# Kernel optimization log

Hardware: AMD Instinct MI355X
Metric: run time of the kernel (lower is better)

The kernel has to match this reference:

```python
import jax, jax.numpy as jnp
import numpy as np


def setup_inputs() -> dict:
    key0 = jax.random.key(0)
    kq, kk, kv = jax.random.split(key0, 3)
    B, S, H, KVH, D = 1, 4096, 8, 2, 64
    return {
        "query": jax.random.normal(kq, (B, S, H, D), dtype=jnp.float32),
        "key": jax.random.normal(kk, (B, S, KVH, D), dtype=jnp.float32),
        "value": jax.random.normal(kv, (B, S, KVH, D), dtype=jnp.float32),
    }


def _ring_attn_single(query, key, value):
    # world_size == 1 (dist uninitialized): ring loop is a single local step
    # with query_offset == key_offset == 0.
    B, S, H, D = query.shape
    KVH = key.shape[2]
    scale = D ** -0.5
    # [B, H, S, D]
    q = query.transpose(0, 2, 1, 3)
    k = key.transpose(0, 2, 1, 3)
    v = value.transpose(0, 2, 1, 3)
    if KVH != H:
        rep = H // KVH
        k = jnp.repeat(k, rep, axis=1)  # repeat_interleave on head dim
        v = jnp.repeat(v, rep, axis=1)
    logits = jnp.einsum("bhqd,bhkd->bhqk", q, k) * scale
    pos = jnp.arange(S)
    causal = pos[:, None] < pos[None, :]  # mask future keys
    logits = jnp.where(causal[None, None], -jnp.inf, logits)
    w = jax.nn.softmax(logits, axis=-1)  # [B, H, S, S]
    attn_out = jnp.einsum("bhqk,bhkd->bhqd", w, v)
    cw = jnp.sum(w, axis=-1, keepdims=True)  # chunk softmax mass (== 1)
    out = attn_out * cw / (cw + 1e-8)  # weight-accumulation renorm
    return out.transpose(0, 2, 1, 3)  # [B, S, H, D]


def reference(query, key, value):
    return _ring_attn_single(query, key, value)
```

## Files before the change

### kernel.cpp

```cpp
#include <hip/hip_runtime.h>
#include <hip/hip_bf16.h>


#define S_LEN 4096
#define H_Q   8
#define H_KV  2
#define DH    64
#define BN    64
#define NEG_BIG (-1e30f)
#define CS (0.125f * 1.44269504088896340736f)

#define CHUNK 6
#define NTR   187
#define KB_SH (S_LEN * H_KV * DH)
#define TILE_SH 4096
#define KVH_SH  (S_LEN * DH)
#define OB_SH    ((size_t)NTR * H_Q * 128 * DH)
#define L_FLOATS ((size_t)NTR * H_Q * 128)
#define WS_NEED ((size_t)(2 * KB_SH) * 2 + OB_SH * 2 + L_FLOATS * 4)

typedef __attribute__((ext_vector_type(8))) short bf16x8;
typedef __attribute__((ext_vector_type(4))) short s16x4;
typedef __attribute__((ext_vector_type(4))) float f32x4;
typedef __attribute__((ext_vector_type(4))) unsigned int u32x4;

__device__ __forceinline__ short bf(float x) {
    return __builtin_bit_cast(short, __float2bfloat16(x));
}
__device__ __forceinline__ float fbf(short u) {
    return __builtin_bit_cast(float, ((unsigned int)(unsigned short)u) << 16);
}
__device__ __forceinline__ unsigned int cvtpk(float lo, float hi) {
    unsigned int r;
    asm("v_cvt_pk_bf16_f32 %0, %1, %2" : "=v"(r) : "v"(lo), "v"(hi));
    return r;
}
__device__ __forceinline__ void gload16(const short* gp, short* lp) {
    __builtin_amdgcn_global_load_lds(
        (const __attribute__((address_space(1))) unsigned int*)gp,
        (__attribute__((address_space(3))) unsigned int*)lp, 16, 0, 0);
}

__global__ __launch_bounds__(256)
void ring_attn_prepass(const float* __restrict__ K, const float* __restrict__ V,
                       short* __restrict__ Kb, short* __restrict__ Vt) {
    const int b = blockIdx.x;
    const int t = threadIdx.x;
    if (b < 512) {
        const int i = (b * 256 + t) * 4;
        const int s   = i >> 7;
        const int kvh = (i >> 6) & 1;
        const int d   = i & 63;
        float4 kv = *(const float4*)(K + i);
        const int dst = kvh * KVH_SH + (s >> 6) * TILE_SH + (s & 63) * 64
                      + (((d >> 3) ^ (s & 7)) * 8) + (d & 7);
        *(unsigned int*)(Kb + dst)     = cvtpk(kv.x, kv.y);
        *(unsigned int*)(Kb + dst + 2) = cvtpk(kv.z, kv.w);
    } else {
        __shared__ short T[DH * 72];
        const int bb  = b - 512;
        const int kvh = bb >> 6;
        const int j   = bb & 63;
        const int s0  = j * 64;
        {
            const int r  = t >> 2;
            const int dq = (t & 3) * 16;
            const float* vp = V + ((s0 + r) * H_KV + kvh) * DH + dq;
            float4 a0 = *(const float4*)(vp);
            float4 a1 = *(const float4*)(vp + 4);
            float4 a2 = *(const float4*)(vp + 8);
            float4 a3 = *(const float4*)(vp + 12);
            float e[16] = {a0.x,a0.y,a0.z,a0.w, a1.x,a1.y,a1.z,a1.w,
                           a2.x,a2.y,a2.z,a2.w, a3.x,a3.y,a3.z,a3.w};
#pragma unroll
            for (int i2 = 0; i2 < 16; ++i2)
                T[(dq + i2) * 72 + r] = bf(e[i2]);
        }
        __syncthreads();
        {
            const int d = t >> 2;
            const int q = t & 3;
            s16x4 g0 = *(const s16x4*)(&T[d * 72 + 4 * q]);
            s16x4 g1 = *(const s16x4*)(&T[d * 72 + 16 + 4 * q]);
            s16x4 g2 = *(const s16x4*)(&T[d * 72 + 32 + 4 * q]);
            s16x4 g3 = *(const s16x4*)(&T[d * 72 + 48 + 4 * q]);
            bf16x8 x0 = bf16x8{g0[0],g0[1],g0[2],g0[3], g1[0],g1[1],g1[2],g1[3]};
            bf16x8 x1 = bf16x8{g2[0],g2[1],g2[2],g2[3], g3[0],g3[1],g3[2],g3[3]};
            short* base = Vt + kvh * KVH_SH + j * TILE_SH + d * 64;
            *(bf16x8*)(base + ((2 * q)     ^ (d & 7)) * 8) = x0;
            *(bf16x8*)(base + ((2 * q + 1) ^ (d & 7)) * 8) = x1;
        }
    }
}

template <bool SPLIT>
__global__ __launch_bounds__(256, 4)
void ring_attn_fwd(const float* __restrict__ Q, const short* __restrict__ Kb,
                   const short* __restrict__ Vt, float* __restrict__ O,
                   short* __restrict__ Obuf, float* __restrict__ Lbuf) {
    const int bid = blockIdx.x;
    const int h   = bid & 7;
    int qt, nch, jbeg, jend, tr0;
    if (SPLIT) {
        const int tr = (NTR - 1) - (bid >> 3);
        int g = 0, base = 0;
        for (;;) {
            const int cnt2 = ((g == 10) ? 2 : 3) * (g + 1);
            if (tr < base + cnt2) break;
            base += cnt2; ++g;
        }
        const int u  = tr - base;
        const int qq = u / (g + 1);
        const int ch = u - qq * (g + 1);
        qt   = 3 * g + qq;
        nch  = g + 1;
        tr0  = base + qq * (g + 1);
        jbeg = ch * CHUNK;
        jend = min(2 * qt + 2, jbeg + CHUNK);
    } else {
        qt = 31 - (bid >> 3);
        nch = 1; jbeg = 0; jend = 2 * qt + 2; tr0 = 0;
    }
    const int kvh = h >> 2;

    __shared__ short Ksb[2][4096];
    __shared__ short Vsb[2][4096];

    const int tid  = threadIdx.x;
    const int w    = tid >> 6;
    const int lane = tid & 63;
    const int c    = lane & 15;
    const int q    = lane >> 4;
    const int e    = c & 7;

    bf16x8 qf[2][2];
#pragma unroll
    for (int st = 0; st < 2; ++st) {
        const int qg = qt * 128 + st * 64 + w * 16 + c;
        const float* qp = Q + (qg * H_Q + h) * DH + q * 8;
        float4 a0 = *(const float4*)(qp);
        float4 a1 = *(const float4*)(qp + 4);
        float4 b0 = *(const float4*)(qp + 32);
        float4 b1 = *(const float4*)(qp + 36);
        u32x4 u0 = {cvtpk(a0.x*CS, a0.y*CS), cvtpk(a0.z*CS, a0.w*CS),
                    cvtpk(a1.x*CS, a1.y*CS), cvtpk(a1.z*CS, a1.w*CS)};
        u32x4 u1 = {cvtpk(b0.x*CS, b0.y*CS), cvtpk(b0.z*CS, b0.w*CS),
                    cvtpk(b1.x*CS, b1.y*CS), cvtpk(b1.z*CS, b1.w*CS)};
        qf[st][0] = __builtin_bit_cast(bf16x8, u0);
        qf[st][1] = __builtin_bit_cast(bf16x8, u1);
    }

    f32x4 acc[2][4] = {};
    float l_lane[2] = {0.f, 0.f};

    const short* gkb = Kb + kvh * KVH_SH + w * 1024 + lane * 8;
    const short* gvb = Vt + kvh * KVH_SH + w * 1024 + lane * 8;
#define STAGE(buf, j)                                             \
    do {                                                          \
        const short* gk = gkb + (j) * TILE_SH;                    \
        const short* gv = gvb + (j) * TILE_SH;                    \
        short* lk = &Ksb[buf][w * 1024];                          \
        short* lv = &Vsb[buf][w * 1024];                          \
        gload16(gk, lk);        gload16(gk + 512, lk + 512);      \
        gload16(gv, lv);        gload16(gv + 512, lv + 512);      \
    } while (0)

    STAGE(0, jbeg);

    for (int j = jbeg; j < jend; ++j) {
        const int cur = (j - jbeg) & 1;
        __syncthreads();
        if (j + 1 < jend)
            STAGE(cur ^ 1, j + 1);

        const short* Kc = Ksb[cur];
        const short* Vc = Vsb[cur];

        f32x4 s[2][4] = {};
#pragma unroll
        for (int nt = 0; nt < 4; ++nt) {
            const int rb = (nt * 16 + c) * 64;
            bf16x8 kf0 = *(const bf16x8*)(Kc + rb + (q ^ e) * 8);
            bf16x8 kf1 = *(const bf16x8*)(Kc + rb + ((q + 4) ^ e) * 8);
            s[0][nt] = __builtin_amdgcn_mfma_f32_16x16x32_bf16(kf0, qf[0][0], s[0][nt], 0, 0, 0);
            s[0][nt] = __builtin_amdgcn_mfma_f32_16x16x32_bf16(kf1, qf[0][1], s[0][nt], 0, 0, 0);
            s[1][nt] = __builtin_amdgcn_mfma_f32_16x16x32_bf16(kf0, qf[1][0], s[1][nt], 0, 0, 0);
            s[1][nt] = __builtin_amdgcn_mfma_f32_16x16x32_bf16(kf1, qf[1][1], s[1][nt], 0, 0, 0);
        }

        bf16x8 pf[2][2];
#pragma unroll
        for (int st = 0; st < 2; ++st) {
            if (j >= 2 * qt + st) {
                const int koff = (j - 2 * qt - st) * 64;
                const int qrl  = w * 16 + c;
#pragma unroll
                for (int nt = 0; nt < 4; ++nt) {
                    const int kl = koff + nt * 16 + q * 4;
#pragma unroll
                    for (int r = 0; r < 4; ++r)
                        if (kl + r > qrl) s[st][nt][r] = NEG_BIG;
                }
            }
#pragma unroll
            for (int nt = 0; nt < 4; ++nt)
#pragma unroll
                for (int r = 0; r < 4; ++r) {
                    const float p = __builtin_amdgcn_exp2f(s[st][nt][r]);
                    s[st][nt][r] = p;
                    l_lane[st] += p;
                }
            u32x4 w0 = {cvtpk(s[st][0][0], s[st][0][1]), cvtpk(s[st][0][2], s[st][0][3]),
                        cvtpk(s[st][1][0], s[st][1][1]), cvtpk(s[st][1][2], s[st][1][3])};
            u32x4 w1 = {cvtpk(s[st][2][0], s[st][2][1]), cvtpk(s[st][2][2], s[st][2][3]),
                        cvtpk(s[st][3][0], s[st][3][1]), cvtpk(s[st][3][2], s[st][3][3])};
            pf[st][0] = __builtin_bit_cast(bf16x8, w0);
            pf[st][1] = __builtin_bit_cast(bf16x8, w1);
        }

#pragma unroll
        for (int dt = 0; dt < 4; ++dt) {
            const int nb = (dt * 16 + c) * 64;
            bf16x8 vf0 = *(const bf16x8*)(Vc + nb + ((2 * q)     ^ e) * 8);
            bf16x8 vf1 = *(const bf16x8*)(Vc + nb + ((2 * q + 1) ^ e) * 8);
            acc[0][dt] = __builtin_amdgcn_mfma_f32_16x16x32_bf16(pf[0][0], vf0, acc[0][dt], 0, 0, 0);
            acc[0][dt] = __builtin_amdgcn_mfma_f32_16x16x32_bf16(pf[0][1], vf1, acc[0][dt], 0, 0, 0);
            acc[1][dt] = __builtin_amdgcn_mfma_f32_16x16x32_bf16(pf[1][0], vf0, acc[1][dt], 0, 0, 0);
            acc[1][dt] = __builtin_amdgcn_mfma_f32_16x16x32_bf16(pf[1][1], vf1, acc[1][dt], 0, 0, 0);
        }
    }

    float lr[2][4];
#pragma unroll
    for (int st = 0; st < 2; ++st) {
        float t2 = l_lane[st];
        t2 += __shfl_xor(t2, 16);
        t2 += __shfl_xor(t2, 32);
        l_lane[st] = t2;
#pragma unroll
        for (int r = 0; r < 4; ++r)
            lr[st][r] = __shfl(t2, q * 4 + r);
    }

    if (!SPLIT || nch == 1) {
#pragma unroll
        for (int st = 0; st < 2; ++st)
#pragma unroll
            for (int r = 0; r < 4; ++r) {
                const float inv = 1.0f / lr[st][r];
                const int row = qt * 128 + st * 64 + w * 16 + q * 4 + r;
                float* op = O + (row * H_Q + h) * DH + c;
#pragma unroll
                for (int dt = 0; dt < 4; ++dt)
                    op[dt * 16] = acc[st][dt][r] * inv;
            }
    } else {
        const int slot = (tr0 + jbeg / CHUNK) * 8 + h;
        short* ob = Obuf + (size_t)slot * (128 * DH);
#pragma unroll
        for (int st = 0; st < 2; ++st) {
#pragma unroll
            for (int r = 0; r < 4; ++r) {
                const int rin = st * 64 + w * 16 + q * 4 + r;
#pragma unroll
                for (int dt = 0; dt < 4; ++dt)
                    ob[rin * DH + dt * 16 + c] = bf(acc[st][dt][r]);
            }
            if (lane < 16)
                Lbuf[slot * 128 + st * 64 + w * 16 + lane] = l_lane[st];
        }
    }
}

__global__ __launch_bounds__(256)
void ring_attn_combine(const short* __restrict__ Obuf, const float* __restrict__ Lbuf,
                       float* __restrict__ O) {
    const int gid  = blockIdx.x * 256 + threadIdx.x;
    const int d    = gid & 63;
    const int h    = (gid >> 6) & 7;
    const int srow = 384 + (gid >> 9);
    const int qt   = srow >> 7;
    const int rin  = srow & 127;
    const int g    = qt / 3;
    const int base = 3 * g * (g + 1) / 2;
    const int nch  = g + 1;
    const int tr0  = base + (qt - 3 * g) * nch;

    float num = 0.0f, den = 0.0f;
    for (int ch = 0; ch < nch; ++ch) {
        const int slot = (tr0 + ch) * 8 + h;
        den += Lbuf[slot * 128 + rin];
        num += fbf(Obuf[(size_t)slot * (128 * DH) + rin * DH + d]);
    }
    O[(srow * H_Q + h) * DH + d] = num / den;
}

extern "C" void kernel_launch(void* const* d_in, const int* in_sizes, int n_in,
                              void* d_out, int out_size, void* d_ws, size_t ws_size,
                              hipStream_t stream) {
    const float* Q = (const float*)d_in[0];
    const float* K = (const float*)d_in[1];
    const float* V = (const float*)d_in[2];
    float* O  = (float*)d_out;
    short* Kb = (short*)d_ws;
    short* Vt = Kb + KB_SH;
    short* Obuf = Vt + KB_SH;
    float* Lbuf = (float*)(Obuf + OB_SH);

    ring_attn_prepass<<<640, 256, 0, stream>>>(K, V, Kb, Vt);
    if (ws_size >= WS_NEED) {
        ring_attn_fwd<true><<<NTR * H_Q, 256, 0, stream>>>(Q, Kb, Vt, O, Obuf, Lbuf);
        ring_attn_combine<<<(S_LEN - 384) * H_Q * DH / 256, 256, 0, stream>>>(Obuf, Lbuf, O);
    } else {
        ring_attn_fwd<false><<<32 * H_Q, 256, 0, stream>>>(Q, Kb, Vt, O, Obuf, Lbuf);
    }
}
```

Baseline: 105.0 us.

## Enlarge split-K chunks to 8 tiles, vectorize combine, split row-sum accumulators

Changes the split-K work decomposition from 6-tile to 8-tile chunks, which gives 144 tile-rows per head, grouped four query tiles per group. The larger chunks mean fewer partial outputs and fewer blocks, at the cost of more work per block and possibly coarser load balance. The combine kernel now has each thread process 8 d-values with bf16x8 loads and float4 stores instead of one scalar per thread. It also uses one reciprocal per row in place of per-element division. The softmax denominator is accumulated in two interleaved partial sums to shorten the dependency chain of the adds.

```diff
diff --git a/kernel.cpp b/kernel.cpp
--- a/kernel.cpp
+++ b/kernel.cpp
@@ -10,8 +10,8 @@
 #define NEG_BIG (-1e30f)
 #define CS (0.125f * 1.44269504088896340736f)
 
-#define CHUNK 6
-#define NTR   187
+#define CHUNK 8
+#define NTR   144
 #define KB_SH (S_LEN * H_KV * DH)
 #define TILE_SH 4096
 #define KVH_SH  (S_LEN * DH)
@@ -105,14 +105,14 @@
         const int tr = (NTR - 1) - (bid >> 3);
         int g = 0, base = 0;
         for (;;) {
-            const int cnt2 = ((g == 10) ? 2 : 3) * (g + 1);
+            const int cnt2 = 4 * (g + 1);
             if (tr < base + cnt2) break;
             base += cnt2; ++g;
         }
         const int u  = tr - base;
         const int qq = u / (g + 1);
         const int ch = u - qq * (g + 1);
-        qt   = 3 * g + qq;
+        qt   = 4 * g + qq;
         nch  = g + 1;
         tr0  = base + qq * (g + 1);
         jbeg = ch * CHUNK;
@@ -151,7 +151,7 @@
     }
 
     f32x4 acc[2][4] = {};
-    float l_lane[2] = {0.f, 0.f};
+    float l_a[2] = {0.f, 0.f}, l_b[2] = {0.f, 0.f};
 
     const short* gkb = Kb + kvh * KVH_SH + w * 1024 + lane * 8;
     const short* gvb = Vt + kvh * KVH_SH + w * 1024 + lane * 8;
@@ -208,7 +208,7 @@
                 for (int r = 0; r < 4; ++r) {
                     const float p = __builtin_amdgcn_exp2f(s[st][nt][r]);
                     s[st][nt][r] = p;
-                    l_lane[st] += p;
+                    if (nt & 1) l_b[st] += p; else l_a[st] += p;
                 }
             u32x4 w0 = {cvtpk(s[st][0][0], s[st][0][1]), cvtpk(s[st][0][2], s[st][0][3]),
                         cvtpk(s[st][1][0], s[st][1][1]), cvtpk(s[st][1][2], s[st][1][3])};
@@ -230,10 +230,10 @@
         }
     }
 
-    float lr[2][4];
+    float lr[2][4], l_lane[2];
 #pragma unroll
     for (int st = 0; st < 2; ++st) {
-        float t2 = l_lane[st];
+        float t2 = l_a[st] + l_b[st];
         t2 += __shfl_xor(t2, 16);
         t2 += __shfl_xor(t2, 32);
         l_lane[st] = t2;
@@ -276,23 +276,30 @@
 void ring_attn_combine(const short* __restrict__ Obuf, const float* __restrict__ Lbuf,
                        float* __restrict__ O) {
     const int gid  = blockIdx.x * 256 + threadIdx.x;
-    const int d    = gid & 63;
-    const int h    = (gid >> 6) & 7;
-    const int srow = 384 + (gid >> 9);
+    const int d0   = (gid & 7) * 8;
+    const int h    = (gid >> 3) & 7;
+    const int srow = 512 + (gid >> 6);
     const int qt   = srow >> 7;
     const int rin  = srow & 127;
-    const int g    = qt / 3;
-    const int base = 3 * g * (g + 1) / 2;
+    const int g    = qt >> 2;
+    const int base = 2 * g * (g + 1);
     const int nch  = g + 1;
-    const int tr0  = base + (qt - 3 * g) * nch;
-
-    float num = 0.0f, den = 0.0f;
+    const int tr0  = base + (qt - 4 * g) * nch;
+
+    float num[8] = {};
+    float den = 0.0f;
     for (int ch = 0; ch < nch; ++ch) {
         const int slot = (tr0 + ch) * 8 + h;
         den += Lbuf[slot * 128 + rin];
-        num += fbf(Obuf[(size_t)slot * (128 * DH) + rin * DH + d]);
-    }
-    O[(srow * H_Q + h) * DH + d] = num / den;
+        bf16x8 v = *(const bf16x8*)(Obuf + (size_t)slot * (128 * DH) + rin * DH + d0);
+#pragma unroll
+        for (int i = 0; i < 8; ++i)
+            num[i] += fbf(v[i]);
+    }
+    const float inv = 1.0f / den;
+    float* op = O + (srow * H_Q + h) * DH + d0;
+    *(float4*)(op)     = float4{num[0]*inv, num[1]*inv, num[2]*inv, num[3]*inv};
+    *(float4*)(op + 4) = float4{num[4]*inv, num[5]*inv, num[6]*inv, num[7]*inv};
 }
 
 extern "C" void kernel_launch(void* const* d_in, const int* in_sizes, int n_in,
@@ -310,7 +317,7 @@
     ring_attn_prepass<<<640, 256, 0, stream>>>(K, V, Kb, Vt);
     if (ws_size >= WS_NEED) {
         ring_attn_fwd<true><<<NTR * H_Q, 256, 0, stream>>>(Q, Kb, Vt, O, Obuf, Lbuf);
-        ring_attn_combine<<<(S_LEN - 384) * H_Q * DH / 256, 256, 0, stream>>>(Obuf, Lbuf, O);
+        ring_attn_combine<<<(S_LEN - 512) * H_Q * DH / 8 / 256, 256, 0, stream>>>(Obuf, Lbuf, O);
     } else {
         ring_attn_fwd<false><<<32 * H_Q, 256, 0, stream>>>(Q, Kb, Vt, O, Obuf, Lbuf);
     }
```

New measurement: 100.9 us (median of 2 runs). -3.9%, faster.
